# Performance work log

Hardware: AMD Instinct MI355X
Metric: run time of the kernel (lower is better)

Reference implementation:

```python
import jax, jax.numpy as jnp
import numpy as np

N = 100000          # nodes
E = 1600000         # edges (avg degree 16)
F_IN, F1, F2, F3, F_OUT = 128, 64, 64, 64, 2
EDGE_DIM = 1
NEG_SLOPE = 0.2     # PyG GATv2Conv default negative_slope


def _init(key, fan_in, shape):
    return jax.random.normal(key, shape, dtype=jnp.float32) / np.float32(np.sqrt(fan_in))


def setup_inputs() -> dict:
    key = jax.random.key(0)
    ks = jax.random.split(key, 24)
    inp = {}
    inp['x'] = jax.random.normal(ks[0], (N, F_IN), dtype=jnp.float32)
    inp['edge_index'] = jax.random.randint(ks[1], (2, E), 0, N, dtype=jnp.int32)
    inp['edge_attr'] = jax.random.uniform(ks[2], (E, EDGE_DIM), dtype=jnp.float32)
    k = 3
    for li, (fi, fo) in enumerate([(F_IN, F1), (F1, F2), (F2, F3)], 1):
        inp[f'Wl{li}'] = _init(ks[k], fi, (fi, fo)); k += 1
        inp[f'bl{li}'] = jnp.zeros((fo,), jnp.float32)
        inp[f'Wr{li}'] = _init(ks[k], fi, (fi, fo)); k += 1
        inp[f'br{li}'] = jnp.zeros((fo,), jnp.float32)
        inp[f'We{li}'] = _init(ks[k], EDGE_DIM, (EDGE_DIM, fo)); k += 1
        inp[f'att{li}'] = _init(ks[k], fo, (fo,)); k += 1
        inp[f'bias{li}'] = jnp.zeros((fo,), jnp.float32)
    inp['W_lin'] = _init(ks[k], F3, (F3, F_OUT)); k += 1
    inp['b_lin'] = jnp.zeros((F_OUT,), jnp.float32)
    return inp


def _gatv2_layer(x, src, dst, ea, Wl, bl, Wr, br, We, att, bias):
    # PyG GATv2Conv, heads=1: x_j = lin_l(x)[src], x_i = lin_r(x)[dst]
    xl = x @ Wl + bl                      # [N, fo] source-side transform
    xr = x @ Wr + br                      # [N, fo] target-side transform
    ee = ea @ We                          # [E+N, fo] edge embedding
    m = xl[src] + xr[dst] + ee            # per-edge message pre-activation
    m = jax.nn.leaky_relu(m, NEG_SLOPE)
    alpha = m @ att                       # [E+N] attention logits
    # segment softmax grouped by destination node (self-loops => no empty segment)
    amax = jax.ops.segment_max(alpha, dst, num_segments=N)
    ex = jnp.exp(alpha - amax[dst])
    denom = jax.ops.segment_sum(ex, dst, num_segments=N)
    w = ex / denom[dst]
    out = jax.ops.segment_sum(xl[src] * w[:, None], dst, num_segments=N)
    return out + bias


def reference(x, edge_index, edge_attr,
              Wl1, bl1, Wr1, br1, We1, att1, bias1,
              Wl2, bl2, Wr2, br2, We2, att2, bias2,
              Wl3, bl3, Wr3, br3, We3, att3, bias3,
              W_lin, b_lin):
    loop = jnp.arange(N, dtype=edge_index.dtype)
    src = jnp.concatenate([edge_index[0], loop])
    dst = jnp.concatenate([edge_index[1], loop])
    # add_self_loops with fill_value='mean' for edge_attr (PyG default)
    ea_mean = jnp.mean(edge_attr, axis=0, keepdims=True)
    ea = jnp.concatenate([edge_attr, jnp.broadcast_to(ea_mean, (N, edge_attr.shape[1]))], axis=0)

    h = _gatv2_layer(x, src, dst, ea, Wl1, bl1, Wr1, br1, We1, att1, bias1)
    h = jax.nn.relu(h)
    h = _gatv2_layer(h, src, dst, ea, Wl2, bl2, Wr2, br2, We2, att2, bias2)
    h = jax.nn.relu(h)
    h = _gatv2_layer(h, src, dst, ea, Wl3, bl3, Wr3, br3, We3, att3, bias3)
    h = jax.nn.relu(h)
    g = jnp.mean(h, axis=0, keepdims=True)   # MeanAggregation over nodes -> [1, F3]
    logits = g @ W_lin + b_lin               # [1, F_OUT]
    return jax.nn.softmax(logits, axis=1)
```

## Files before the change

### kernel.cpp

```cpp
#include <hip/hip_runtime.h>
#include <hip/hip_bf16.h>

#define NNODES 100000
#define NEDGES 1600000
#define NEG_SLOPE 0.2f

#define CHUNK 4096
#define EPT 16
#define NBLK ((NEDGES + CHUNK - 1) / CHUNK)
#define NB ((NNODES + 255) / 256)
#define FLATN (NB * NBLK)
#define SCB ((FLATN + 255) / 256)
#define FCAP 5632

typedef __attribute__((ext_vector_type(8))) short bf16x8;
typedef __attribute__((ext_vector_type(4))) float f32x4;

__device__ __forceinline__ float wave_sum64(float v) {
#pragma unroll
    for (int off = 1; off < 64; off <<= 1) v += __shfl_xor(v, off, 64);
    return v;
}

__device__ __forceinline__ int wave_sum64i(int v) {
#pragma unroll
    for (int off = 1; off < 64; off <<= 1) v += __shfl_xor(v, off, 64);
    return v;
}

__device__ __forceinline__ unsigned short bf16rne(float a) {
    unsigned u = __float_as_uint(a);
    return (unsigned short)((u + 0x7FFFu + ((u >> 16) & 1u)) >> 16);
}

__device__ __forceinline__ unsigned pack_bf2(float a, float b) {
    unsigned ua = __float_as_uint(a), ub = __float_as_uint(b);
    ua = (ua + 0x7FFFu + ((ua >> 16) & 1u)) >> 16;
    ub = (ub + 0x7FFFu + ((ub >> 16) & 1u));
    return ua | (ub & 0xFFFF0000u);
}

__device__ __forceinline__ void unpack_bf8(uint4 w, float* f) {
    f[0] = __uint_as_float(w.x << 16);
    f[1] = __uint_as_float(w.x & 0xFFFF0000u);
    f[2] = __uint_as_float(w.y << 16);
    f[3] = __uint_as_float(w.y & 0xFFFF0000u);
    f[4] = __uint_as_float(w.z << 16);
    f[5] = __uint_as_float(w.z & 0xFFFF0000u);
    f[6] = __uint_as_float(w.w << 16);
    f[7] = __uint_as_float(w.w & 0xFFFF0000u);
}


__global__ __launch_bounds__(256) void k_lsort(const int* __restrict__ src,
                                               const int* __restrict__ dst,
                                               const float* __restrict__ ea,
                                               uint2* __restrict__ tmps,
                                               int* __restrict__ gcnt,
                                               int* __restrict__ lscan,
                                               float* __restrict__ easum) {
    __shared__ uint2 ent[CHUNK];
    __shared__ unsigned short perm[CHUNK];
    __shared__ int hist[NB];
    __shared__ int cur[NB];
    __shared__ float ws[4];
    const int t = threadIdx.x;
    const int j = blockIdx.x;
    const int base = j * CHUNK;
    const int n = min(CHUNK, NEDGES - base);

    for (int b = t; b < NB; b += 256) hist[b] = 0;
    __syncthreads();

    int bkt[EPT];
    float s = 0.f;
#pragma unroll
    for (int k = 0; k < EPT; ++k) {
        const int l = t + k * 256;
        bkt[k] = -1;
        if (l < n) {
            const int i = base + l;
            const int d = dst[i];
            const float e = ea[i];
            const int b = d >> 8;
            bkt[k] = b;
            ent[l] = make_uint2((unsigned)src[i] | ((unsigned)(d & 255) << 17),
                                __float_as_uint(e));
            atomicAdd(&hist[b], 1);
            s += e;
        }
    }
    s = wave_sum64(s);
    if ((t & 63) == 0) ws[t >> 6] = s;
    __syncthreads();
    if (t == 0) atomicAdd(easum, ws[0] + ws[1] + ws[2] + ws[3]);

    if (t < 64) {
        int x[7];
        int run = 0;
#pragma unroll
        for (int q = 0; q < 7; ++q) {
            const int idx = t * 7 + q;
            x[q] = (idx < NB) ? hist[idx] : 0;
            run += x[q];
        }
        int inc = run;
#pragma unroll
        for (int o = 1; o < 64; o <<= 1) {
            int u = __shfl_up(inc, o, 64);
            if (t >= o) inc += u;
        }
        int r = inc - run;
#pragma unroll
        for (int q = 0; q < 7; ++q) {
            const int idx = t * 7 + q;
            if (idx < NB) cur[idx] = r;
            r += x[q];
        }
    }
    __syncthreads();

#pragma unroll
    for (int k = 0; k < EPT; ++k) {
        if (bkt[k] >= 0) {
            const int r = atomicAdd(&cur[bkt[k]], 1);
            perm[r] = (unsigned short)(t + k * 256);
        }
    }
    __syncthreads();

    for (int o = t; o < n; o += 256)
        tmps[base + o] = ent[perm[o]];
    for (int b = t; b < NB; b += 256) {
        gcnt[b * NBLK + j] = hist[b];
        lscan[j * NB + b] = cur[b] - hist[b];
    }
}


__global__ __launch_bounds__(256) void k_part2(const int* __restrict__ v, int n,
                                               int* __restrict__ bsum) {
    int i = blockIdx.x * 256 + threadIdx.x;
    int x = (i < n) ? v[i] : 0;
    x = wave_sum64i(x);
    __shared__ int wsh[4];
    if ((threadIdx.x & 63) == 0) wsh[threadIdx.x >> 6] = x;
    __syncthreads();
    if (threadIdx.x == 0) bsum[blockIdx.x] = wsh[0] + wsh[1] + wsh[2] + wsh[3];
}

__global__ __launch_bounds__(1024) void k_scanb2(const int* __restrict__ bsum, int nb,
                                                 int* __restrict__ boff,
                                                 int* __restrict__ rowptr) {
    __shared__ int sh[1024];
    int t = threadIdx.x;
    int v = (t < nb) ? bsum[t] : 0;
    sh[t] = v;
    __syncthreads();
    for (int off = 1; off < 1024; off <<= 1) {
        int u = (t >= off) ? sh[t - off] : 0;
        __syncthreads();
        sh[t] += u;
        __syncthreads();
    }
    if (t < nb) boff[t] = sh[t] - v;
    if (t == 0) rowptr[NNODES] = NEDGES;
}

__global__ __launch_bounds__(256) void k_scanfin2(const int* __restrict__ v, int n,
                                                  const int* __restrict__ boff,
                                                  int* __restrict__ out) {
    int t = threadIdx.x, lane = t & 63, wave = t >> 6;
    int i = blockIdx.x * 256 + t;
    int x = (i < n) ? v[i] : 0;
    int orig = x;
#pragma unroll
    for (int off = 1; off < 64; off <<= 1) {
        int u = __shfl_up(x, off, 64);
        if (lane >= off) x += u;
    }
    __shared__ int wsh[4];
    if (lane == 63) wsh[wave] = x;
    __syncthreads();
    int wexc = 0;
    for (int w = 0; w < wave; ++w) wexc += wsh[w];
    if (i < n) out[i] = boff[blockIdx.x] + wexc + x - orig;
}


__global__ __launch_bounds__(256) void k_fsort(const uint2* __restrict__ tmps,
                                               const int* __restrict__ lscan,
                                               const int* __restrict__ goff,
                                               int* __restrict__ rowptr,
                                               uint2* __restrict__ edata) {
    __shared__ uint2 ent[FCAP];
    __shared__ unsigned short perm[FCAP];
    __shared__ int joff[NBLK + 1];
    __shared__ int jsrc[NBLK];
    __shared__ int hist[256];
    __shared__ int cur[256];
    const int b = blockIdx.x;
    const int t = threadIdx.x;
    const int base = goff[b * NBLK];

    for (int q = t; q < 256; q += 256) hist[q] = 0;
    for (int j = t; j < NBLK; j += 256) {
        joff[j] = goff[b * NBLK + j] - base;
        jsrc[j] = j * CHUNK + lscan[j * NB + b];
    }
    if (t == 0) joff[NBLK] = ((b == NB - 1) ? NEDGES : goff[(b + 1) * NBLK]) - base;
    __syncthreads();
    const int T = min(joff[NBLK], FCAP);

    for (int idx = t; idx < T; idx += 256) {
        int lo = 0, hi = NBLK;
        while (hi - lo > 1) { int mid = (lo + hi) >> 1; if (joff[mid] <= idx) lo = mid; else hi = mid; }
        const uint2 e = tmps[jsrc[lo] + (idx - joff[lo])];
        ent[idx] = e;
        atomicAdd(&hist[(e.x >> 17) & 255u], 1);
    }
    __syncthreads();

    if (t < 64) {
        int x[4];
        int run = 0;
#pragma unroll
        for (int q = 0; q < 4; ++q) { x[q] = hist[t * 4 + q]; run += x[q]; }
        int inc = run;
#pragma unroll
        for (int o = 1; o < 64; o <<= 1) {
            int u = __shfl_up(inc, o, 64);
            if (t >= o) inc += u;
        }
        int r = inc - run;
#pragma unroll
        for (int q = 0; q < 4; ++q) { cur[t * 4 + q] = r; r += x[q]; }
    }
    __syncthreads();

    {
        const int i = b * 256 + t;
        if (i < NNODES) rowptr[i] = base + cur[t];
    }
    __syncthreads();

    for (int idx = t; idx < T; idx += 256) {
        const int d = (int)((ent[idx].x >> 17) & 255u);
        const int r = atomicAdd(&cur[d], 1);
        perm[r] = (unsigned short)idx;
    }
    __syncthreads();
    for (int k = t; k < T; k += 256)
        edata[base + k] = ent[perm[k]];
}


__global__ __launch_bounds__(256) void k_wprep(const float* __restrict__ W1l, const float* __restrict__ W1r,
                                               const float* __restrict__ W2l, const float* __restrict__ W2r,
                                               const float* __restrict__ W3l, const float* __restrict__ W3r,
                                               unsigned short* __restrict__ Wt1,
                                               unsigned short* __restrict__ Wt2,
                                               unsigned short* __restrict__ Wt3) {
    const int idx = blockIdx.x * 256 + threadIdx.x;
    if (idx < 16384) {
        const int c = idx >> 7, k = idx & 127;
        const float v = (c < 64) ? W1l[k * 64 + c] : W1r[k * 64 + (c - 64)];
        Wt1[c * 128 + k] = bf16rne(v);
    } else if (idx < 24576) {
        const int j = idx - 16384;
        const int c = j >> 6, k = j & 63;
        const float v = (c < 64) ? W2l[k * 64 + c] : W2r[k * 64 + (c - 64)];
        Wt2[c * 64 + k] = bf16rne(v);
    } else if (idx < 32768) {
        const int j = idx - 24576;
        const int c = j >> 6, k = j & 63;
        const float v = (c < 64) ? W3l[k * 64 + c] : W3r[k * 64 + (c - 64)];
        Wt3[c * 64 + k] = bf16rne(v);
    }
}


template <int K, bool F32IN>
__global__ __launch_bounds__(256) void k_gemm_mfma(const void* __restrict__ Xin,
                                                   const unsigned short* __restrict__ Wt,
                                                   const float* __restrict__ bl,
                                                   const float* __restrict__ br,
                                                   unsigned short* __restrict__ XLu,
                                                   unsigned short* __restrict__ XRu) {
    constexpr int KP = K + 8;
    __shared__ unsigned short sA[64 * KP];
    __shared__ unsigned short sB[128 * KP];
    const int t = threadIdx.x;
    const int w = t >> 6, lane = t & 63;
    const int r0 = blockIdx.x * 64;

    {
        const uint4* Wu = (const uint4*)Wt;
#pragma unroll
        for (int idx = t; idx < 128 * (K / 8); idx += 256) {
            const int row = idx / (K / 8), q = idx % (K / 8);
            *(uint4*)&sB[row * KP + q * 8] = Wu[idx];
        }
    }
    if constexpr (F32IN) {
        const float* X = (const float*)Xin;
        for (int idx = t; idx < 64 * (K / 4); idx += 256) {
            const int row = idx / (K / 4), q = idx % (K / 4);
            const int rr = min(r0 + row, NNODES - 1);
            const float4 v = *(const float4*)&X[(size_t)rr * K + q * 4];
            unsigned* p = (unsigned*)&sA[row * KP + q * 4];
            p[0] = pack_bf2(v.x, v.y);
            p[1] = pack_bf2(v.z, v.w);
        }
    } else {
        const uint4* X = (const uint4*)Xin;
        for (int idx = t; idx < 64 * 8; idx += 256) {
            const int row = idx >> 3, q = idx & 7;
            const int rr = min(r0 + row, NNODES - 1);
            *(uint4*)&sA[row * KP + q * 8] = X[(size_t)rr * 8 + q];
        }
    }
    __syncthreads();

    f32x4 acc[8] = {};
    const int mrow = w * 16 + (lane & 15);
    const int kb = (lane >> 4) * 8;
#pragma unroll
    for (int kc = 0; kc < K / 32; ++kc) {
        const bf16x8 af = *(const bf16x8*)&sA[mrow * KP + kc * 32 + kb];
#pragma unroll
        for (int nt = 0; nt < 8; ++nt) {
            const bf16x8 bfr = *(const bf16x8*)&sB[(nt * 16 + (lane & 15)) * KP + kc * 32 + kb];
            acc[nt] = __builtin_amdgcn_mfma_f32_16x16x32_bf16(af, bfr, acc[nt], 0, 0, 0);
        }
    }

    const int colL = lane & 15;
    const int rbase = r0 + w * 16 + (lane >> 4) * 4;
#pragma unroll
    for (int nt = 0; nt < 8; ++nt) {
        const int col = nt * 16 + colL;
        const bool isL = col < 64;
        const float bv = isL ? bl[col] : br[col - 64];
        unsigned short* OUT = isL ? XLu : XRu;
        const int oc = isL ? col : col - 64;
#pragma unroll
        for (int r = 0; r < 4; ++r) {
            const int grow = rbase + r;
            if (grow < NNODES)
                OUT[(size_t)grow * 64 + oc] = bf16rne(acc[nt][r] + bv);
        }
    }
}


__global__ __launch_bounds__(256) void k_edge(const uint4* __restrict__ XLh,
                                              const uint4* __restrict__ XRh,
                                              const int* __restrict__ rowptr,
                                              const uint2* __restrict__ edata,
                                              const float* __restrict__ We,
                                              const float* __restrict__ att,
                                              const float* __restrict__ bias,
                                              const float* __restrict__ easum,
                                              unsigned* __restrict__ Hh) {
    __shared__ float red[4][8][65];
    const int wave = threadIdx.x >> 6, lane = threadIdx.x & 63;
    const int g = lane >> 3, fl = lane & 7;
    const int fo = fl * 8;
    float We8[8], att8[8];
    *(float4*)&We8[0] = *(const float4*)&We[fo];
    *(float4*)&We8[4] = *(const float4*)&We[fo + 4];
    *(float4*)&att8[0] = *(const float4*)&att[fo];
    *(float4*)&att8[4] = *(const float4*)&att[fo + 4];
    const float bias_l = bias[lane];
    const float ea_mean = easum[0] * (1.0f / NEDGES);

    const int i = blockIdx.x * 4 + wave;

    float xr8[8], xl8[8], acc8[8];
    unpack_bf8(XRh[(size_t)i * 8 + fl], xr8);
    unpack_bf8(XLh[(size_t)i * 8 + fl], xl8);

    float M;
    {
        float s1 = 0.f, s2 = 0.f;
#pragma unroll
        for (int f = 0; f < 8; ++f) {
            const float m = fmaf(ea_mean, We8[f], xr8[f]) + xl8[f];
            s1 = fmaf(att8[f], m, s1);
            s2 = fmaf(att8[f], fabsf(m), s2);
        }
        float pt = fmaf(0.6f, s1, 0.4f * s2);
        pt += __shfl_xor(pt, 1);
        pt += __shfl_xor(pt, 2);
        pt += __shfl_xor(pt, 4);
        M = pt;
    }
    float S = (g == 0) ? 1.f : 0.f;
#pragma unroll
    for (int f = 0; f < 8; ++f) acc8[f] = (g == 0) ? xl8[f] : 0.f;

    const int e0 = rowptr[i];
    const int ne = rowptr[i + 1] - e0;
    const uint2 z2 = make_uint2(0u, 0u);

    uint2 se = (g < ne) ? edata[e0 + g] : z2;
    for (int e = 0; e < ne; e += 8) {
        const uint2 se_cur = se;
        const bool valid = (e + g) < ne;
        if (e + 8 + g < ne) se = edata[e0 + e + 8 + g];
        const int s = (int)(se_cur.x & 0x1FFFFu);
        const float eav = __uint_as_float(se_cur.y);
        float v8[8];
        unpack_bf8(XLh[(size_t)s * 8 + fl], v8);

        float s1 = 0.f, s2 = 0.f;
#pragma unroll
        for (int f = 0; f < 8; ++f) {
            const float m = fmaf(eav, We8[f], xr8[f]) + v8[f];
            s1 = fmaf(att8[f], m, s1);
            s2 = fmaf(att8[f], fabsf(m), s2);
        }
        float d = fmaf(0.6f, s1, 0.4f * s2);
        d += __shfl_xor(d, 1);
        d += __shfl_xor(d, 2);
        d += __shfl_xor(d, 4);
        const float a = valid ? d : -1e30f;

        const float p = __expf(a - M);
        S += p;
#pragma unroll
        for (int f = 0; f < 8; ++f) acc8[f] = fmaf(p, v8[f], acc8[f]);
    }

    S += __shfl_xor(S, 8);
    S += __shfl_xor(S, 16);
    S += __shfl_xor(S, 32);

#pragma unroll
    for (int k = 0; k < 8; ++k) red[wave][g][fo + k] = acc8[k];
    asm volatile("" ::: "memory");
    __builtin_amdgcn_wave_barrier();
    float o = 0.f;
#pragma unroll
    for (int gg = 0; gg < 8; ++gg) o += red[wave][gg][lane];
    o = fmaxf(o / S + bias_l, 0.f);
    const float on = __shfl_xor(o, 1);
    if (!(lane & 1))
        Hh[(size_t)i * 32 + (lane >> 1)] = pack_bf2(o, on);
}


__global__ __launch_bounds__(256) void k_colsum(const unsigned* __restrict__ Hh,
                                                float* __restrict__ gsum) {
    const int t = threadIdx.x;
    const int c = t & 31;
    const int rl = t >> 5;
    float s0 = 0.f, s1 = 0.f;
    for (int r = blockIdx.x * 8 + rl; r < NNODES; r += gridDim.x * 8) {
        const unsigned u = Hh[(size_t)r * 32 + c];
        s0 += __uint_as_float(u << 16);
        s1 += __uint_as_float(u & 0xFFFF0000u);
    }
    __shared__ float ls[8][64];
    ls[rl][2 * c] = s0;
    ls[rl][2 * c + 1] = s1;
    __syncthreads();
    if (t < 64) {
        float s = 0.f;
#pragma unroll
        for (int q = 0; q < 8; ++q) s += ls[q][t];
        atomicAdd(&gsum[t], s);
    }
}

__global__ __launch_bounds__(64) void k_head(const float* __restrict__ gsum,
                                             const float* __restrict__ Wlin,
                                             const float* __restrict__ blin,
                                             float* __restrict__ out) {
    int lane = threadIdx.x;
    float g = gsum[lane] * (1.0f / NNODES);
    float a0 = wave_sum64(g * Wlin[lane * 2 + 0]);
    float a1 = wave_sum64(g * Wlin[lane * 2 + 1]);
    if (lane == 0) {
        float l0 = a0 + blin[0], l1 = a1 + blin[1];
        float mx = fmaxf(l0, l1);
        float e0 = __expf(l0 - mx), e1 = __expf(l1 - mx);
        float inv = 1.f / (e0 + e1);
        out[0] = e0 * inv;
        out[1] = e1 * inv;
    }
}

extern "C" void kernel_launch(void* const* d_in, const int* in_sizes, int n_in,
                              void* d_out, int out_size, void* d_ws, size_t ws_size,
                              hipStream_t stream) {
    const float* x = (const float*)d_in[0];
    const int* ei = (const int*)d_in[1];
    const float* ea = (const float*)d_in[2];
    const int* src = ei;
    const int* dst = ei + NEDGES;
    auto W = [&](int i) { return (const float*)d_in[i]; };

    char* ws = (char*)d_ws;
    size_t off = 0;
    auto alloc = [&](size_t bytes) {
        void* p = ws + off;
        off += (bytes + 255) & ~(size_t)255;
        return p;
    };
    unsigned short* XLu = (unsigned short*)alloc((size_t)NNODES * 64 * 2);
    unsigned short* XRu = (unsigned short*)alloc((size_t)NNODES * 64 * 2);
    unsigned* Hh = (unsigned*)alloc((size_t)NBLK * CHUNK * 8);
    int* rowptr = (int*)alloc((size_t)(NNODES + 1) * 4);
    uint2* edata = (uint2*)alloc((size_t)NEDGES * 8);
    float* easum = (float*)alloc(4);
    float* gsum = (float*)alloc(64 * 4);
    int* gcnt = (int*)alloc((size_t)FLATN * 4);
    int* lscan = (int*)alloc((size_t)FLATN * 4);
    int* goff = (int*)alloc((size_t)FLATN * 4);
    int* part2 = (int*)alloc((size_t)SCB * 4);
    int* boff2 = (int*)alloc((size_t)SCB * 4);
    unsigned short* Wt1 = (unsigned short*)alloc(16384 * 2);
    unsigned short* Wt2 = (unsigned short*)alloc(8192 * 2);
    unsigned short* Wt3 = (unsigned short*)alloc(8192 * 2);
    uint2* tmps = (uint2*)Hh;

    hipMemsetAsync(easum, 0, 4, stream);
    hipMemsetAsync(gsum, 0, 64 * 4, stream);

    k_wprep<<<128, 256, 0, stream>>>(W(3), W(5), W(10), W(12), W(17), W(19), Wt1, Wt2, Wt3);
    k_lsort<<<NBLK, 256, 0, stream>>>(src, dst, ea, tmps, gcnt, lscan, easum);
    k_part2<<<SCB, 256, 0, stream>>>(gcnt, FLATN, part2);
    k_scanb2<<<1, 1024, 0, stream>>>(part2, SCB, boff2, rowptr);
    k_scanfin2<<<SCB, 256, 0, stream>>>(gcnt, FLATN, boff2, goff);
    k_fsort<<<NB, 256, 0, stream>>>(tmps, lscan, goff, rowptr, edata);

    int gemm_grid = (NNODES + 63) / 64;
    int edge_grid = NNODES / 4;

    k_gemm_mfma<128, true><<<gemm_grid, 256, 0, stream>>>(x, Wt1, W(4), W(6), XLu, XRu);
    k_edge<<<edge_grid, 256, 0, stream>>>((const uint4*)XLu, (const uint4*)XRu, rowptr, edata,
                                          W(7), W(8), W(9), easum, Hh);
    k_gemm_mfma<64, false><<<gemm_grid, 256, 0, stream>>>(Hh, Wt2, W(11), W(13), XLu, XRu);
    k_edge<<<edge_grid, 256, 0, stream>>>((const uint4*)XLu, (const uint4*)XRu, rowptr, edata,
                                          W(14), W(15), W(16), easum, Hh);
    k_gemm_mfma<64, false><<<gemm_grid, 256, 0, stream>>>(Hh, Wt3, W(18), W(20), XLu, XRu);
    k_edge<<<edge_grid, 256, 0, stream>>>((const uint4*)XLu, (const uint4*)XRu, rowptr, edata,
                                          W(21), W(22), W(23), easum, Hh);

    k_colsum<<<256, 256, 0, stream>>>(Hh, gsum);
    k_head<<<1, 64, 0, stream>>>(gsum, W(24), W(25), (float*)d_out);
}
```

Measured before the change: 306.7 us.

## Switch intermediate storage and edge attention math from bf16 to packed fp16

Replaces bf16 storage of node features and weights with fp16 and uses the fp16 MFMA for the linear transforms. The per-edge attention logit now runs in packed half2 FMAs, with the 0.6/0.4 leaky-relu factors folded into precomputed attention vectors. This is meant to halve the ALU work in the edge loop and drop the bf16 unpack shifts. The trade-off is fp16 range limits and fp16 accumulation of the attention dot products, which loses some accuracy.

```diff
diff --git a/kernel.cpp b/kernel.cpp
--- a/kernel.cpp
+++ b/kernel.cpp
@@ -13,7 +13,8 @@
 #define SCB ((FLATN + 255) / 256)
 #define FCAP 5632
 
-typedef __attribute__((ext_vector_type(8))) short bf16x8;
+typedef __attribute__((ext_vector_type(8))) _Float16 f16x8;
+typedef __attribute__((ext_vector_type(2))) _Float16 h2;
 typedef __attribute__((ext_vector_type(4))) float f32x4;
 
 __device__ __forceinline__ float wave_sum64(float v) {
@@ -28,27 +29,27 @@
     return v;
 }
 
-__device__ __forceinline__ unsigned short bf16rne(float a) {
-    unsigned u = __float_as_uint(a);
-    return (unsigned short)((u + 0x7FFFu + ((u >> 16) & 1u)) >> 16);
-}
-
-__device__ __forceinline__ unsigned pack_bf2(float a, float b) {
-    unsigned ua = __float_as_uint(a), ub = __float_as_uint(b);
-    ua = (ua + 0x7FFFu + ((ua >> 16) & 1u)) >> 16;
-    ub = (ub + 0x7FFFu + ((ub >> 16) & 1u));
-    return ua | (ub & 0xFFFF0000u);
-}
-
-__device__ __forceinline__ void unpack_bf8(uint4 w, float* f) {
-    f[0] = __uint_as_float(w.x << 16);
-    f[1] = __uint_as_float(w.x & 0xFFFF0000u);
-    f[2] = __uint_as_float(w.y << 16);
-    f[3] = __uint_as_float(w.y & 0xFFFF0000u);
-    f[4] = __uint_as_float(w.z << 16);
-    f[5] = __uint_as_float(w.z & 0xFFFF0000u);
-    f[6] = __uint_as_float(w.w << 16);
-    f[7] = __uint_as_float(w.w & 0xFFFF0000u);
+__device__ __forceinline__ unsigned short f16rne(float a) {
+    _Float16 h = (_Float16)a;
+    unsigned short u;
+    __builtin_memcpy(&u, &h, 2);
+    return u;
+}
+
+__device__ __forceinline__ unsigned packh2(float a, float b) {
+    h2 v = {(_Float16)a, (_Float16)b};
+    unsigned u;
+    __builtin_memcpy(&u, &v, 4);
+    return u;
+}
+
+__device__ __forceinline__ h2 habs(h2 x) {
+    unsigned u;
+    __builtin_memcpy(&u, &x, 4);
+    u &= 0x7FFF7FFFu;
+    h2 r;
+    __builtin_memcpy(&r, &u, 4);
+    return r;
 }
 
 
@@ -265,17 +266,17 @@
     if (idx < 16384) {
         const int c = idx >> 7, k = idx & 127;
         const float v = (c < 64) ? W1l[k * 64 + c] : W1r[k * 64 + (c - 64)];
-        Wt1[c * 128 + k] = bf16rne(v);
+        Wt1[c * 128 + k] = f16rne(v);
     } else if (idx < 24576) {
         const int j = idx - 16384;
         const int c = j >> 6, k = j & 63;
         const float v = (c < 64) ? W2l[k * 64 + c] : W2r[k * 64 + (c - 64)];
-        Wt2[c * 64 + k] = bf16rne(v);
+        Wt2[c * 64 + k] = f16rne(v);
     } else if (idx < 32768) {
         const int j = idx - 24576;
         const int c = j >> 6, k = j & 63;
         const float v = (c < 64) ? W3l[k * 64 + c] : W3r[k * 64 + (c - 64)];
-        Wt3[c * 64 + k] = bf16rne(v);
+        Wt3[c * 64 + k] = f16rne(v);
     }
 }
 
@@ -309,8 +310,8 @@
             const int rr = min(r0 + row, NNODES - 1);
             const float4 v = *(const float4*)&X[(size_t)rr * K + q * 4];
             unsigned* p = (unsigned*)&sA[row * KP + q * 4];
-            p[0] = pack_bf2(v.x, v.y);
-            p[1] = pack_bf2(v.z, v.w);
+            p[0] = packh2(v.x, v.y);
+            p[1] = packh2(v.z, v.w);
         }
     } else {
         const uint4* X = (const uint4*)Xin;
@@ -327,11 +328,11 @@
     const int kb = (lane >> 4) * 8;
 #pragma unroll
     for (int kc = 0; kc < K / 32; ++kc) {
-        const bf16x8 af = *(const bf16x8*)&sA[mrow * KP + kc * 32 + kb];
+        const f16x8 af = *(const f16x8*)&sA[mrow * KP + kc * 32 + kb];
 #pragma unroll
         for (int nt = 0; nt < 8; ++nt) {
-            const bf16x8 bfr = *(const bf16x8*)&sB[(nt * 16 + (lane & 15)) * KP + kc * 32 + kb];
-            acc[nt] = __builtin_amdgcn_mfma_f32_16x16x32_bf16(af, bfr, acc[nt], 0, 0, 0);
+            const f16x8 bfr = *(const f16x8*)&sB[(nt * 16 + (lane & 15)) * KP + kc * 32 + kb];
+            acc[nt] = __builtin_amdgcn_mfma_f32_16x16x32_f16(af, bfr, acc[nt], 0, 0, 0);
         }
     }
 
@@ -348,7 +349,7 @@
         for (int r = 0; r < 4; ++r) {
             const int grow = rbase + r;
             if (grow < NNODES)
-                OUT[(size_t)grow * 64 + oc] = bf16rne(acc[nt][r] + bv);
+                OUT[(size_t)grow * 64 + oc] = f16rne(acc[nt][r] + bv);
         }
     }
 }
@@ -367,38 +368,52 @@
     const int wave = threadIdx.x >> 6, lane = threadIdx.x & 63;
     const int g = lane >> 3, fl = lane & 7;
     const int fo = fl * 8;
-    float We8[8], att8[8];
-    *(float4*)&We8[0] = *(const float4*)&We[fo];
-    *(float4*)&We8[4] = *(const float4*)&We[fo + 4];
-    *(float4*)&att8[0] = *(const float4*)&att[fo];
-    *(float4*)&att8[4] = *(const float4*)&att[fo + 4];
+    h2 We2[4], a06[4], a04[4];
+#pragma unroll
+    for (int k = 0; k < 4; ++k) {
+        We2[k] = h2{(_Float16)We[fo + 2 * k], (_Float16)We[fo + 2 * k + 1]};
+        a06[k] = h2{(_Float16)(0.6f * att[fo + 2 * k]), (_Float16)(0.6f * att[fo + 2 * k + 1])};
+        a04[k] = h2{(_Float16)(0.4f * att[fo + 2 * k]), (_Float16)(0.4f * att[fo + 2 * k + 1])};
+    }
     const float bias_l = bias[lane];
     const float ea_mean = easum[0] * (1.0f / NEDGES);
 
     const int i = blockIdx.x * 4 + wave;
 
-    float xr8[8], xl8[8], acc8[8];
-    unpack_bf8(XRh[(size_t)i * 8 + fl], xr8);
-    unpack_bf8(XLh[(size_t)i * 8 + fl], xl8);
+    h2 xr2[4], xl2[4];
+    {
+        const uint4 wr = XRh[(size_t)i * 8 + fl];
+        __builtin_memcpy(xr2, &wr, 16);
+        const uint4 wl = XLh[(size_t)i * 8 + fl];
+        __builtin_memcpy(xl2, &wl, 16);
+    }
 
     float M;
     {
-        float s1 = 0.f, s2 = 0.f;
-#pragma unroll
-        for (int f = 0; f < 8; ++f) {
-            const float m = fmaf(ea_mean, We8[f], xr8[f]) + xl8[f];
-            s1 = fmaf(att8[f], m, s1);
-            s2 = fmaf(att8[f], fabsf(m), s2);
-        }
-        float pt = fmaf(0.6f, s1, 0.4f * s2);
+        const _Float16 eh = (_Float16)ea_mean;
+        const h2 ev2 = h2{eh, eh};
+        h2 s1v = h2{(_Float16)0.f, (_Float16)0.f};
+        h2 s2v = s1v;
+#pragma unroll
+        for (int k = 0; k < 4; ++k) {
+            const h2 m = __builtin_elementwise_fma(ev2, We2[k], xr2[k]) + xl2[k];
+            s1v = __builtin_elementwise_fma(a06[k], m, s1v);
+            s2v = __builtin_elementwise_fma(a04[k], habs(m), s2v);
+        }
+        const h2 sv = s1v + s2v;
+        float pt = (float)sv[0] + (float)sv[1];
         pt += __shfl_xor(pt, 1);
         pt += __shfl_xor(pt, 2);
         pt += __shfl_xor(pt, 4);
         M = pt;
     }
     float S = (g == 0) ? 1.f : 0.f;
-#pragma unroll
-    for (int f = 0; f < 8; ++f) acc8[f] = (g == 0) ? xl8[f] : 0.f;
+    float acc8[8];
+#pragma unroll
+    for (int k = 0; k < 4; ++k) {
+        acc8[2 * k] = (g == 0) ? (float)xl2[k][0] : 0.f;
+        acc8[2 * k + 1] = (g == 0) ? (float)xl2[k][1] : 0.f;
+    }
 
     const int e0 = rowptr[i];
     const int ne = rowptr[i + 1] - e0;
@@ -411,17 +426,22 @@
         if (e + 8 + g < ne) se = edata[e0 + e + 8 + g];
         const int s = (int)(se_cur.x & 0x1FFFFu);
         const float eav = __uint_as_float(se_cur.y);
-        float v8[8];
-        unpack_bf8(XLh[(size_t)s * 8 + fl], v8);
-
-        float s1 = 0.f, s2 = 0.f;
-#pragma unroll
-        for (int f = 0; f < 8; ++f) {
-            const float m = fmaf(eav, We8[f], xr8[f]) + v8[f];
-            s1 = fmaf(att8[f], m, s1);
-            s2 = fmaf(att8[f], fabsf(m), s2);
-        }
-        float d = fmaf(0.6f, s1, 0.4f * s2);
+        const uint4 wv = XLh[(size_t)s * 8 + fl];
+        h2 v2[4];
+        __builtin_memcpy(v2, &wv, 16);
+        const _Float16 eh = (_Float16)eav;
+        const h2 ev2 = h2{eh, eh};
+
+        h2 s1v = h2{(_Float16)0.f, (_Float16)0.f};
+        h2 s2v = s1v;
+#pragma unroll
+        for (int k = 0; k < 4; ++k) {
+            const h2 m = __builtin_elementwise_fma(ev2, We2[k], xr2[k]) + v2[k];
+            s1v = __builtin_elementwise_fma(a06[k], m, s1v);
+            s2v = __builtin_elementwise_fma(a04[k], habs(m), s2v);
+        }
+        const h2 sv = s1v + s2v;
+        float d = (float)sv[0] + (float)sv[1];
         d += __shfl_xor(d, 1);
         d += __shfl_xor(d, 2);
         d += __shfl_xor(d, 4);
@@ -430,7 +450,10 @@
         const float p = __expf(a - M);
         S += p;
 #pragma unroll
-        for (int f = 0; f < 8; ++f) acc8[f] = fmaf(p, v8[f], acc8[f]);
+        for (int k = 0; k < 4; ++k) {
+            acc8[2 * k] = fmaf(p, (float)v2[k][0], acc8[2 * k]);
+            acc8[2 * k + 1] = fmaf(p, (float)v2[k][1], acc8[2 * k + 1]);
+        }
     }
 
     S += __shfl_xor(S, 8);
@@ -447,7 +470,7 @@
     o = fmaxf(o / S + bias_l, 0.f);
     const float on = __shfl_xor(o, 1);
     if (!(lane & 1))
-        Hh[(size_t)i * 32 + (lane >> 1)] = pack_bf2(o, on);
+        Hh[(size_t)i * 32 + (lane >> 1)] = packh2(o, on);
 }
 
 
@@ -459,8 +482,10 @@
     float s0 = 0.f, s1 = 0.f;
     for (int r = blockIdx.x * 8 + rl; r < NNODES; r += gridDim.x * 8) {
         const unsigned u = Hh[(size_t)r * 32 + c];
-        s0 += __uint_as_float(u << 16);
-        s1 += __uint_as_float(u & 0xFFFF0000u);
+        h2 hv;
+        __builtin_memcpy(&hv, &u, 4);
+        s0 += (float)hv[0];
+        s1 += (float)hv[1];
     }
     __shared__ float ls[8][64];
     ls[rl][2 * c] = s0;
```

Result: faster. 297.0 us (-3.2%).
